# Optimization experiments

Measured on AMD Instinct MI355X. Metric: run time of the kernel, lower is better.

The kernel has to match this reference:

```python
import jax, jax.numpy as jnp
import numpy as np

M, K, N = 1024, 8192, 8192
PACK = 16  # 16 two-bit codes per int32 word


def _pack_ternary(codes):
    # codes: (N, K) int32 with values in {0,1,3} -> (N, K//16) int32
    c = codes.reshape(N, K // PACK, PACK).astype(jnp.uint32)
    shifts = (jnp.arange(PACK, dtype=jnp.uint32) * 2)
    packed = jnp.sum(c << shifts, axis=-1, dtype=jnp.uint32)
    return jax.lax.bitcast_convert_type(packed, jnp.int32)


def setup_inputs() -> dict:
    key = jax.random.key(0)
    kx, kw, kb = jax.random.split(key, 3)
    x = jax.random.normal(kx, (M, K), dtype=jnp.float16)
    # ternary codes drawn from {0,1,3} (code 2 is unused by the format)
    vals = jnp.array([0, 1, 3], dtype=jnp.int32)
    codes = vals[jax.random.randint(kw, (N, K), 0, 3)]
    packed_w = _pack_ternary(codes)
    bias = jax.random.normal(kb, (N,), dtype=jnp.float16)
    return {"x": x, "packed_w": packed_w, "bias": bias}


def _unpack(packed_w):
    # (N, K//16) int32 -> (N, K) fp16 weights with values in {0,1,3}
    shifts = jnp.arange(PACK, dtype=jnp.int32) * 2
    w = (packed_w[:, :, None] >> shifts) & 3  # mask keeps low 2 bits even with arithmetic shift
    return w.reshape(packed_w.shape[0], -1).astype(jnp.float16)


def reference(x, packed_w, bias):
    w = _unpack(packed_w)  # (N, K)
    # Y = X W^T + b, fp32 accumulation as in the CUDA/Triton GEMM, fp16 output
    y = jnp.einsum('mk,nk->mn', x, w, preferred_element_type=jnp.float32)
    y = y.astype(jnp.float16) + bias
    return y
```

## Files before the change

### kernel.cpp

```cpp
#include <hip/hip_runtime.h>
#include <hip/hip_fp16.h>
#include <stdint.h>

#define M_DIM 1024
#define N_DIM 8192
#define K_DIM 8192
#define KP    (K_DIM / 16)

#define BM 128
#define BN 128
#define BK 64
#define NTHREADS 256
#define B_STRIDE 144

#define MT_STRIDE 2097152
#define KT_STRIDE 16384

typedef _Float16 half8   __attribute__((ext_vector_type(8)));
typedef __fp16   fp16x2  __attribute__((ext_vector_type(2)));
typedef float    f32x4   __attribute__((ext_vector_type(4)));
typedef float    f32x16  __attribute__((ext_vector_type(16)));

__device__ __forceinline__ uint32_t cvt2(float a, float b) {
  fp16x2 p = __builtin_amdgcn_cvt_pkrtz(a, b);
  return __builtin_bit_cast(uint32_t, p);
}

__device__ __forceinline__ void gload_lds16(const char* g, char* l) {
  __builtin_amdgcn_global_load_lds(
      (const __attribute__((address_space(1))) void*)g,
      (__attribute__((address_space(3))) void*)l, 16, 0, 0);
}

__device__ __forceinline__ half8 dec_frag(uint32_t word, uint32_t sh) {
  const uint32_t T = 0x42063C00u;
  uint32_t h  = (word >> sh) & 0xFFFFu;
  uint32_t W  = (h & 0x3333u) | ((h << 14) & 0x33330000u);
  uint32_t c0 = __builtin_amdgcn_perm(0u, W, 0x04040200u);
  uint32_t c1 = __builtin_amdgcn_perm(0u, W, 0x04040301u);
  uint32_t s0 = (c0 * 0x1001u) & 0x03030303u;
  uint32_t s1 = (c1 * 0x1001u) & 0x03030303u;
  uint32_t P0 = __builtin_amdgcn_perm(0u, T, s0);
  uint32_t P1 = __builtin_amdgcn_perm(0u, T, s1);
  uint4 v;
  v.x = __builtin_amdgcn_perm(P0, 0u, 0x05000400u);
  v.y = __builtin_amdgcn_perm(P0, 0u, 0x07000600u);
  v.z = __builtin_amdgcn_perm(P1, 0u, 0x05000400u);
  v.w = __builtin_amdgcn_perm(P1, 0u, 0x07000600u);
  return __builtin_bit_cast(half8, v);
}

__global__ __launch_bounds__(256)
void cvt_x_t(const float* __restrict__ x, char* __restrict__ xhT) {
  __shared__ __align__(16) char st[16384];
  const int b  = blockIdx.x;
  const int mt = b >> 7, kt = b & 127;
  const int t  = threadIdx.x;
#pragma unroll
  for (int p = 0; p < 8; ++p) {
    int f   = t + 256 * p;
    int R   = f >> 4;
    int cc4 = f & 15;
    float4 v = *(const float4*)(x + (size_t)(mt * 128 + R) * K_DIM + kt * 64 + cc4 * 4);
    uint32_t w0 = cvt2(v.x, v.y), w1 = cvt2(v.z, v.w);
    int c8 = cc4 >> 1, hh = cc4 & 1;
    int i32 = R >> 5, r = R & 31, ks = c8 >> 1, q = c8 & 1;
    *(uint2*)(st + i32 * 4096 + ks * 1024 + q * 512 + r * 16 + hh * 8) = make_uint2(w0, w1);
  }
  __syncthreads();
  char* outb = xhT + (size_t)mt * MT_STRIDE + (size_t)kt * KT_STRIDE;
#pragma unroll
  for (int e = 0; e < 4; ++e) {
    int d = (e * 256 + t) * 16;
    *(uint4*)(outb + d) = *(const uint4*)(st + d);
  }
}

__global__ __launch_bounds__(NTHREADS, 2)
void ternary_gemm_dc(const char* __restrict__ xhT,
                     const int*  __restrict__ pw,
                     const float* __restrict__ bias,
                     float*       __restrict__ out) {
  __shared__ __align__(16) char Ast[2 * 16384];
  __shared__ __align__(16) char stg[2 * 2048];

  const int tid  = threadIdx.x;
  const int lane = tid & 63;
  const int w    = tid >> 6;
  const int wm   = w >> 1, wn = w & 1;
  const int bid  = blockIdx.x;
  const int mt   = bid & 7;
  const int bm   = mt * BM;
  const int bn   = (bid >> 3) * BN;

  const char* gAs = xhT + (size_t)mt * MT_STRIDE + w * 4096 + lane * 16;
  char* const lA0 = Ast + w * 4096;
  char* const lA1 = Ast + 16384 + w * 4096;

  const int rT = tid >> 1, hT = tid & 1;
  const int2* gB = (const int2*)pw + (size_t)(bn + rT) * (KP / 2) + hT;
  const int stOff = rT * 16 + hT * 8;

  int rowOff[2];
#pragma unroll
  for (int j = 0; j < 2; ++j)
    rowOff[j] = (wn * 64 + j * 32 + (lane & 31)) * 16;
  const uint32_t sh = (lane >> 5) * 16;

  const char* const aPtr = Ast + wm * 8192 + lane * 16;

  f32x16 acc[2][2];
#pragma unroll
  for (int i = 0; i < 2; ++i)
#pragma unroll
    for (int j = 0; j < 2; ++j) acc[i][j] = (f32x16)(0.f);

  const int NT = K_DIM / BK;

  auto stageA = [&](char* lbase, int kt) {
    const char* g = gAs + (size_t)kt * KT_STRIDE;
#pragma unroll
    for (int e = 0; e < 4; ++e)
      gload_lds16(g + e * 1024, lbase + e * 1024);
  };

  stageA(lA0, 0);
  *(int2*)(stg + stOff) = gB[0];
  int2 wcur = gB[2];
  __syncthreads();

  auto step = [&](int cur, int kt) {
    if (kt + 1 < NT) stageA(cur ? lA0 : lA1, kt + 1);

    uint32_t wr0[4], wr1[4];
    *(uint4*)wr0 = *(const uint4*)(stg + cur * 2048 + rowOff[0]);
    *(uint4*)wr1 = *(const uint4*)(stg + cur * 2048 + rowOff[1]);
    *(int2*)(stg + (cur ^ 1) * 2048 + stOff) = wcur;
    int kn2 = (kt + 2 < NT) ? (kt + 2) : (NT - 1);
    int2 wnxt = gB[kn2 * 2];

#pragma unroll
    for (int ks = 0; ks < 4; ++ks) {
      half8 a0 = *(const half8*)(aPtr + cur * 16384 + 0 * 4096 + ks * 1024);
      half8 a1 = *(const half8*)(aPtr + cur * 16384 + 1 * 4096 + ks * 1024);
      half8 bf0 = dec_frag(wr0[ks], sh);
      half8 bf1 = dec_frag(wr1[ks], sh);
      acc[0][0] = __builtin_amdgcn_mfma_f32_32x32x16_f16(a0, bf0, acc[0][0], 0, 0, 0);
      acc[0][1] = __builtin_amdgcn_mfma_f32_32x32x16_f16(a0, bf1, acc[0][1], 0, 0, 0);
      acc[1][0] = __builtin_amdgcn_mfma_f32_32x32x16_f16(a1, bf0, acc[1][0], 0, 0, 0);
      acc[1][1] = __builtin_amdgcn_mfma_f32_32x32x16_f16(a1, bf1, acc[1][1], 0, 0, 0);
    }

    __syncthreads();
    wcur = wnxt;
  };

  for (int kt = 0; kt < NT; kt += 2) {
    step(0, kt);
    step(1, kt + 1);
  }

#pragma unroll
  for (int j = 0; j < 2; ++j) {
    int n = bn + wn * 64 + j * 32 + (lane & 31);
    __half hb = __float2half_rn(bias[n]);
#pragma unroll
    for (int i = 0; i < 2; ++i) {
      int mbase = bm + wm * 64 + i * 32 + 4 * (lane >> 5);
#pragma unroll
      for (int reg = 0; reg < 16; ++reg) {
        int m = mbase + (reg & 3) + 8 * (reg >> 2);
        __half hy = __float2half_rn(acc[i][j][reg]);
        out[(size_t)m * N_DIM + n] = __half2float(__hadd(hy, hb));
      }
    }
  }
}

__device__ __forceinline__ uint32_t unpack_pair16(uint32_t u, int p) {
  uint32_t c0 = (u >> (4 * p)) & 3u;
  uint32_t c1 = (u >> (4 * p + 2)) & 3u;
  uint32_t lo = (c0 & 1u) * 0x3C00u + (c0 >> 1) * 0x0600u;
  uint32_t hi = (c1 & 1u) * 0x3C00u + (c1 >> 1) * 0x0600u;
  return lo | (hi << 16);
}

__global__ __launch_bounds__(NTHREADS, 2)
void ternary_gemm(const float* __restrict__ x,
                  const int*   __restrict__ pw,
                  const float* __restrict__ bias,
                  float*       __restrict__ out) {
  __shared__ __align__(16) char AsB[128 * B_STRIDE];
  __shared__ __align__(16) char BsB[128 * B_STRIDE];

  const int tid  = threadIdx.x;
  const int lane = tid & 63;
  const int w    = tid >> 6;
  const int wm   = w >> 1, wn = w & 1;
  const int bid  = blockIdx.x;
  const int bm   = (bid & 7) * 128;
  const int bn   = (bid >> 3) * 128;

  const int rT = tid >> 1, hT = tid & 1;
  const float* gA = x + (size_t)(bm + rT) * K_DIM + hT * 32;
  char* const  lA = AsB + rT * B_STRIDE + hT * 64;
  const int2* gB = (const int2*)pw + (size_t)(bn + rT) * (KP / 2) + hT;
  char* dBp[4];
#pragma unroll
  for (int h = 0; h < 4; ++h)
    dBp[h] = BsB + rT * B_STRIDE + (hT * 4 + h) * 16;

  int offA[4][2], offB[4][2];
#pragma unroll
  for (int i = 0; i < 4; ++i)
#pragma unroll
    for (int ks = 0; ks < 2; ++ks) {
      int c = ks * 4 + (lane >> 4);
      offA[i][ks] = (wm * 64 + i * 16 + (lane & 15)) * B_STRIDE + c * 16;
      offB[i][ks] = (wn * 64 + i * 16 + (lane & 15)) * B_STRIDE + c * 16;
    }

  f32x4 acc[4][4];
#pragma unroll
  for (int i = 0; i < 4; ++i)
#pragma unroll
    for (int j = 0; j < 4; ++j)
      acc[i][j] = (f32x4){0.f, 0.f, 0.f, 0.f};

  const int NT = K_DIM / BK;
  for (int kt = 0; kt < NT; ++kt) {
    __syncthreads();
    int2 wcur = gB[kt * 2];
    float4 av[8];
#pragma unroll
    for (int v = 0; v < 8; ++v) av[v] = *(const float4*)(gA + kt * BK + v * 4);
    uint32_t d0[8], d1[8];
#pragma unroll
    for (int p = 0; p < 8; ++p) d0[p] = unpack_pair16((uint32_t)wcur.x, p);
#pragma unroll
    for (int p = 0; p < 8; ++p) d1[p] = unpack_pair16((uint32_t)wcur.y, p);
    *(uint4*)dBp[0] = make_uint4(d0[0], d0[1], d0[2], d0[3]);
    *(uint4*)dBp[1] = make_uint4(d0[4], d0[5], d0[6], d0[7]);
    *(uint4*)dBp[2] = make_uint4(d1[0], d1[1], d1[2], d1[3]);
    *(uint4*)dBp[3] = make_uint4(d1[4], d1[5], d1[6], d1[7]);
#pragma unroll
    for (int v = 0; v < 4; ++v) {
      uint4 aw;
      aw.x = cvt2(av[2 * v].x, av[2 * v].y);
      aw.y = cvt2(av[2 * v].z, av[2 * v].w);
      aw.z = cvt2(av[2 * v + 1].x, av[2 * v + 1].y);
      aw.w = cvt2(av[2 * v + 1].z, av[2 * v + 1].w);
      *(uint4*)(lA + v * 16) = aw;
    }
    __syncthreads();
#pragma unroll
    for (int ks = 0; ks < 2; ++ks) {
      half8 af[4], bf[4];
#pragma unroll
      for (int i = 0; i < 4; ++i) af[i] = *(const half8*)(AsB + offA[i][ks]);
#pragma unroll
      for (int j = 0; j < 4; ++j) bf[j] = *(const half8*)(BsB + offB[j][ks]);
#pragma unroll
      for (int i = 0; i < 4; ++i)
#pragma unroll
        for (int j = 0; j < 4; ++j)
          acc[i][j] = __builtin_amdgcn_mfma_f32_16x16x32_f16(af[i], bf[j], acc[i][j], 0, 0, 0);
    }
  }
#pragma unroll
  for (int j = 0; j < 4; ++j) {
    int n = bn + wn * 64 + j * 16 + (lane & 15);
    __half hb = __float2half_rn(bias[n]);
#pragma unroll
    for (int i = 0; i < 4; ++i) {
      int m0 = bm + wm * 64 + i * 16 + (lane >> 4) * 4;
#pragma unroll
      for (int r = 0; r < 4; ++r) {
        __half hy = __float2half_rn(acc[i][j][r]);
        out[(size_t)(m0 + r) * N_DIM + n] = __half2float(__hadd(hy, hb));
      }
    }
  }
}

extern "C" void kernel_launch(void* const* d_in, const int* in_sizes, int n_in,
                              void* d_out, int out_size, void* d_ws, size_t ws_size,
                              hipStream_t stream) {
  (void)in_sizes; (void)n_in; (void)out_size;
  const float* x    = (const float*)d_in[0];
  const int*   pwp  = (const int*)d_in[1];
  const float* bias = (const float*)d_in[2];
  float*       outp = (float*)d_out;

  const size_t need = (size_t)M_DIM * K_DIM * 2;
  if (ws_size >= need) {
    char* xhT = (char*)d_ws;
    cvt_x_t<<<8 * 128, 256, 0, stream>>>(x, xhT);
    dim3 grid((M_DIM / BM) * (N_DIM / BN));
    ternary_gemm_dc<<<grid, NTHREADS, 0, stream>>>(xhT, pwp, bias, outp);
  } else {
    dim3 grid((M_DIM / 128) * (N_DIM / 128));
    ternary_gemm<<<grid, NTHREADS, 0, stream>>>(x, pwp, bias, outp);
  }
}
```

Measured before the change: 240.5 us.

## Triple-buffer A tiles and use counted vmcnt waits instead of full syncthreads

Moves the A-tile LDS staging from a double buffer to a triple buffer, so loads for tile kt+2 are issued while tile kt is computed. The block barrier in steady state now waits only until at most five vector memory ops are outstanding rather than draining them all, which should keep prefetches in flight across the barrier. This raises LDS use per block (about 54KB), which may limit occupancy at two blocks per CU. The hand-tuned vmcnt count and the modulo-3 buffer indexing are fragile if the number of loads per step changes.

```diff
diff --git a/kernel.cpp b/kernel.cpp
--- a/kernel.cpp
+++ b/kernel.cpp
@@ -81,8 +81,8 @@
                      const int*  __restrict__ pw,
                      const float* __restrict__ bias,
                      float*       __restrict__ out) {
-  __shared__ __align__(16) char Ast[2 * 16384];
-  __shared__ __align__(16) char stg[2 * 2048];
+  __shared__ __align__(16) char Ast[3 * 16384];
+  __shared__ __align__(16) char stg[3 * 2048];
 
   const int tid  = threadIdx.x;
   const int lane = tid & 63;
@@ -94,8 +94,6 @@
   const int bn   = (bid >> 3) * BN;
 
   const char* gAs = xhT + (size_t)mt * MT_STRIDE + w * 4096 + lane * 16;
-  char* const lA0 = Ast + w * 4096;
-  char* const lA1 = Ast + 16384 + w * 4096;
 
   const int rT = tid >> 1, hT = tid & 1;
   const int2* gB = (const int2*)pw + (size_t)(bn + rT) * (KP / 2) + hT;
@@ -117,27 +115,31 @@
 
   const int NT = K_DIM / BK;
 
-  auto stageA = [&](char* lbase, int kt) {
+  auto stageA = [&](int buf, int kt) {
     const char* g = gAs + (size_t)kt * KT_STRIDE;
+    char* lbase = Ast + buf * 16384 + w * 4096;
 #pragma unroll
     for (int e = 0; e < 4; ++e)
       gload_lds16(g + e * 1024, lbase + e * 1024);
   };
 
-  stageA(lA0, 0);
-  *(int2*)(stg + stOff) = gB[0];
+  stageA(0, 0);
+  stageA(1, 1);
+  int2 w0 = gB[0];
+  *(int2*)(stg + stOff) = w0;
   int2 wcur = gB[2];
   __syncthreads();
 
-  auto step = [&](int cur, int kt) {
-    if (kt + 1 < NT) stageA(cur ? lA0 : lA1, kt + 1);
+  int2 wnxt;
+  auto step = [&](int cur, int kt, bool counted) {
+    if (kt + 2 < NT) stageA((cur + 2) % 3, kt + 2);
 
     uint32_t wr0[4], wr1[4];
     *(uint4*)wr0 = *(const uint4*)(stg + cur * 2048 + rowOff[0]);
     *(uint4*)wr1 = *(const uint4*)(stg + cur * 2048 + rowOff[1]);
-    *(int2*)(stg + (cur ^ 1) * 2048 + stOff) = wcur;
+    *(int2*)(stg + ((cur + 1) % 3) * 2048 + stOff) = wcur;
     int kn2 = (kt + 2 < NT) ? (kt + 2) : (NT - 1);
-    int2 wnxt = gB[kn2 * 2];
+    wnxt = gB[kn2 * 2];
 
 #pragma unroll
     for (int ks = 0; ks < 4; ++ks) {
@@ -151,14 +153,25 @@
       acc[1][1] = __builtin_amdgcn_mfma_f32_32x32x16_f16(a1, bf1, acc[1][1], 0, 0, 0);
     }
 
-    __syncthreads();
+    if (counted) {
+      __builtin_amdgcn_sched_barrier(0);
+      asm volatile("s_waitcnt vmcnt(5) lgkmcnt(0)" ::: "memory");
+      __builtin_amdgcn_s_barrier();
+      asm volatile("" ::: "memory");
+      __builtin_amdgcn_sched_barrier(0);
+    } else {
+      __syncthreads();
+    }
     wcur = wnxt;
   };
 
-  for (int kt = 0; kt < NT; kt += 2) {
-    step(0, kt);
-    step(1, kt + 1);
-  }
+  for (int kt = 0; kt < NT - 2; kt += 3) {
+    step(0, kt, true);
+    step(1, kt + 1, true);
+    step(2, kt + 2, true);
+  }
+  step(0, NT - 2, false);
+  step(1, NT - 1, false);
 
 #pragma unroll
   for (int j = 0; j < 2; ++j) {
```

New measurement: 234.5 us. -2.5%, faster.
